# Kernel tuning notes

Measured on AMD Instinct MI355X. Metric: run time of the kernel, lower is better.

The kernel has to match this reference:

```python
import jax, jax.numpy as jnp
import numpy as np
from jax import lax

B, S, CIN, COUT, K = 32, 2048, 256, 256, 16


def setup_inputs() -> dict:
    key = jax.random.key(0)
    k1, k2, k3, k4 = jax.random.split(key, 4)
    x = jax.random.normal(k1, (B, S, CIN), dtype=jnp.float32)
    w_real = jax.random.normal(k2, (COUT, CIN, K), dtype=jnp.float32) * 0.1
    w_imag = jax.random.normal(k3, (COUT, CIN, K), dtype=jnp.float32) * 0.1
    phases = jax.random.normal(k4, (K,), dtype=jnp.float32) * 0.1
    return {"x": x, "w_real": w_real, "w_imag": w_imag, "phases": phases}


def reference(x, w_real, w_imag, phases):
    # out[b,t,o] = Re( sum_{k,i} x[b,t+k,i] * exp(1j*phases[k]) * (w_real + 1j*w_imag)[o,i,k] )
    # x is real, so this equals a real valid conv1d with effective kernel:
    #   w_eff[o,i,k] = cos(phases[k]) * w_real[o,i,k] - sin(phases[k]) * w_imag[o,i,k]
    w_eff = jnp.cos(phases)[None, None, :] * w_real - jnp.sin(phases)[None, None, :] * w_imag
    # conv expects NCH / OIH layouts
    y = lax.conv_general_dilated(
        jnp.transpose(x, (0, 2, 1)),  # [B, CIN, S]
        w_eff,                         # [COUT, CIN, K]
        window_strides=(1,),
        padding="VALID",
        dimension_numbers=("NCH", "OIH", "NCH"),
    )
    return jnp.transpose(y, (0, 2, 1))  # [B, S-K+1, COUT]
```

## Files before the change

kernel.cpp:

```cpp
#include <hip/hip_runtime.h>
#include <math.h>

#define B_    32
#define S_    2048
#define CIN_  256
#define COUT_ 256
#define K_    16
#define TOUT_ 2033
#define RTOT_ 4096

typedef __bf16 bf16x4 __attribute__((ext_vector_type(4)));
typedef __bf16 bf16x8 __attribute__((ext_vector_type(8)));
typedef float  f32x4  __attribute__((ext_vector_type(4)));

#define GLOBAL_AS __attribute__((address_space(1)))
#define LDS_AS    __attribute__((address_space(3)))

__device__ __forceinline__ void gload_lds16(const void* g, void* l) {
  __builtin_amdgcn_global_load_lds((const GLOBAL_AS void*)g, (LDS_AS void*)l, 16, 0, 0);
}

__global__ void __launch_bounds__(256) build_wt_kernel(const float* __restrict__ wr,
                                                       const float* __restrict__ wi,
                                                       const float* __restrict__ ph,
                                                       __bf16* __restrict__ wt) {
  int t = blockIdx.x * 256 + threadIdx.x;
  int o = t >> 8, i = t & 255;
  const float4* wr4 = (const float4*)(wr + (size_t)(o * CIN_ + i) * K_);
  const float4* wi4 = (const float4*)(wi + (size_t)(o * CIN_ + i) * K_);
  float re[16], im[16];
  #pragma unroll
  for (int v = 0; v < 4; v++) {
    float4 a = wr4[v];
    re[4*v+0]=a.x; re[4*v+1]=a.y; re[4*v+2]=a.z; re[4*v+3]=a.w;
    float4 b = wi4[v];
    im[4*v+0]=b.x; im[4*v+1]=b.y; im[4*v+2]=b.z; im[4*v+3]=b.w;
  }
  #pragma unroll
  for (int kk = 0; kk < K_; kk++) {
    float p = ph[kk];
    wt[(size_t)o * RTOT_ + kk * CIN_ + i] = (__bf16)(cosf(p)*re[kk] - sinf(p)*im[kk]);
  }
}

__global__ void __launch_bounds__(256) conv_mfma_kernel(const float* __restrict__ xg,
                                                        const __bf16* __restrict__ wt,
                                                        float* __restrict__ out) {
  __shared__ __align__(16) __bf16 As[144 * 32];
  __shared__ __align__(16) __bf16 Bs[128 * 32];

  const int bx = blockIdx.x;
  const int nb = bx & 1;
  const int mb = (bx >> 1) & 15;
  const int b  = bx >> 5;

  const int tid  = threadIdx.x;
  const int w    = tid >> 6;
  const int lane = tid & 63;
  const int wm   = w >> 1, wn = w & 1;
  const int n16  = lane & 15, q = lane >> 4;

  const int t0 = mb * 128;
  const int o0 = nb * 128;

  const float* xbase = xg + (size_t)b * (S_ * CIN_);

  const int sr = tid >> 3;
  const int sc = (tid & 7) * 4;
  const int br = w * 16 + (lane >> 2);
  const int bc = (lane & 3) * 8;

  f32x4 acc[4][4];
  #pragma unroll
  for (int im_ = 0; im_ < 4; im_++)
    #pragma unroll
    for (int in_ = 0; in_ < 4; in_++)
      acc[im_][in_] = {0.f, 0.f, 0.f, 0.f};

  for (int ic = 0; ic < 8; ++ic) {
    const int i0 = ic * 32;

    __syncthreads();

    {
      const float* xcol = xbase + i0 + sc;
      #pragma unroll
      for (int p = 0; p < 4; p++) {
        int r = p * 32 + sr;
        int rg = t0 + r; rg = (rg < S_) ? rg : (S_ - 1);
        float4 v = *(const float4*)(xcol + (size_t)rg * CIN_);
        bf16x4 o4; o4[0]=(__bf16)v.x; o4[1]=(__bf16)v.y; o4[2]=(__bf16)v.z; o4[3]=(__bf16)v.w;
        *(bf16x4*)(As + r * 32 + sc) = o4;
      }
      if (tid < 128) {
        int r = 128 + sr;
        int rg = t0 + r; rg = (rg < S_) ? rg : (S_ - 1);
        float4 v = *(const float4*)(xcol + (size_t)rg * CIN_);
        bf16x4 o4; o4[0]=(__bf16)v.x; o4[1]=(__bf16)v.y; o4[2]=(__bf16)v.z; o4[3]=(__bf16)v.w;
        *(bf16x4*)(As + r * 32 + sc) = o4;
      }
    }

    for (int kk = 0; kk < K_; ++kk) {
      if (kk) __syncthreads();

      const __bf16* wcol = wt + (size_t)kk * CIN_ + i0 + bc;
      #pragma unroll
      for (int p = 0; p < 2; p++) {
        int orow = o0 + p * 64 + br;
        gload_lds16(wcol + (size_t)orow * RTOT_,
                    (void*)(Bs + (p * 64 + w * 16) * 32));
      }

      __syncthreads();

      bf16x8 af[4], bfrag[4];
      #pragma unroll
      for (int jm = 0; jm < 4; jm++) {
        int row = kk + wm * 64 + jm * 16 + n16;
        af[jm] = *(const bf16x8*)(As + row * 32 + q * 8);
      }
      #pragma unroll
      for (int jn = 0; jn < 4; jn++) {
        int row = wn * 64 + jn * 16 + n16;
        bfrag[jn] = *(const bf16x8*)(Bs + row * 32 + q * 8);
      }
      #pragma unroll
      for (int jm = 0; jm < 4; jm++)
        #pragma unroll
        for (int jn = 0; jn < 4; jn++)
          acc[jm][jn] = __builtin_amdgcn_mfma_f32_16x16x32_bf16(af[jm], bfrag[jn], acc[jm][jn], 0, 0, 0);
    }
  }

  float* obase = out + (size_t)b * TOUT_ * COUT_;
  #pragma unroll
  for (int jm = 0; jm < 4; jm++) {
    #pragma unroll
    for (int r = 0; r < 4; r++) {
      int t = t0 + wm * 64 + jm * 16 + q * 4 + r;
      if (t < TOUT_) {
        float* orow = obase + (size_t)t * COUT_ + o0 + wn * 64 + n16;
        #pragma unroll
        for (int jn = 0; jn < 4; jn++)
          orow[jn * 16] = acc[jm][jn][r];
      }
    }
  }
}

extern "C" void kernel_launch(void* const* d_in, const int* in_sizes, int n_in,
                              void* d_out, int out_size, void* d_ws, size_t ws_size,
                              hipStream_t stream) {
  const float* x  = (const float*)d_in[0];
  const float* wr = (const float*)d_in[1];
  const float* wi = (const float*)d_in[2];
  const float* ph = (const float*)d_in[3];
  float* out = (float*)d_out;

  __bf16* wt = (__bf16*)d_ws;

  build_wt_kernel<<<dim3((COUT_ * CIN_) / 256), dim3(256), 0, stream>>>(wr, wi, ph, wt);
  conv_mfma_kernel<<<dim3(B_ * 16 * 2), dim3(256), 0, stream>>>(x, wt, out);
}
```

Baseline: 230.2 us.

## Pipeline weight tiles through a 4-deep LDS ring with async prefetch

Flattens the channel-chunk and tap loops into one 128-step loop. Weight tiles are prefetched two steps ahead into a 4-buffer LDS ring using global_load_lds, and the two barriers per step become a single hand-written s_waitcnt vmcnt + s_barrier. The aim is to hide weight-load latency behind the MFMA work and cut synchronisation. It also raises MFMA wave priority with s_setprio and asks for 3 blocks per CU through launch bounds. The risks are that hand-counted vmcnt values can be upset by compiler-inserted waits around the input-tile loads, and the larger LDS footprint plus the register cap could cause spills or lower occupancy.

```diff
diff --git a/kernel.cpp b/kernel.cpp
--- a/kernel.cpp
+++ b/kernel.cpp
@@ -43,11 +43,11 @@
   }
 }
 
-__global__ void __launch_bounds__(256) conv_mfma_kernel(const float* __restrict__ xg,
-                                                        const __bf16* __restrict__ wt,
-                                                        float* __restrict__ out) {
+__global__ void __launch_bounds__(256, 3) conv_mfma_kernel(const float* __restrict__ xg,
+                                                           const __bf16* __restrict__ wt,
+                                                           float* __restrict__ out) {
   __shared__ __align__(16) __bf16 As[144 * 32];
-  __shared__ __align__(16) __bf16 Bs[128 * 32];
+  __shared__ __align__(16) __bf16 Bs[4][128 * 32];
 
   const int bx = blockIdx.x;
   const int nb = bx & 1;
@@ -77,59 +77,75 @@
     for (int in_ = 0; in_ < 4; in_++)
       acc[im_][in_] = {0.f, 0.f, 0.f, 0.f};
 
-  for (int ic = 0; ic < 8; ++ic) {
-    const int i0 = ic * 32;
+  auto stage_a = [&](int ic) {
+    const float* xcol = xbase + ic * 32 + sc;
+    #pragma unroll
+    for (int p = 0; p < 4; p++) {
+      int r = p * 32 + sr;
+      int rg = t0 + r; rg = (rg < S_) ? rg : (S_ - 1);
+      float4 v = *(const float4*)(xcol + (size_t)rg * CIN_);
+      bf16x4 o4; o4[0]=(__bf16)v.x; o4[1]=(__bf16)v.y; o4[2]=(__bf16)v.z; o4[3]=(__bf16)v.w;
+      *(bf16x4*)(As + r * 32 + sc) = o4;
+    }
+    if (tid < 128) {
+      int r = 128 + sr;
+      int rg = t0 + r; rg = (rg < S_) ? rg : (S_ - 1);
+      float4 v = *(const float4*)(xcol + (size_t)rg * CIN_);
+      bf16x4 o4; o4[0]=(__bf16)v.x; o4[1]=(__bf16)v.y; o4[2]=(__bf16)v.z; o4[3]=(__bf16)v.w;
+      *(bf16x4*)(As + r * 32 + sc) = o4;
+    }
+  };
 
-    __syncthreads();
+  auto stage_b = [&](int j) {
+    const int kk = j & 15;
+    const int i0 = (j >> 4) * 32;
+    const __bf16* wcol = wt + (size_t)kk * CIN_ + i0 + bc;
+    __bf16* dst = &Bs[j & 3][(w * 16) * 32];
+    #pragma unroll
+    for (int p = 0; p < 2; p++) {
+      int orow = o0 + p * 64 + br;
+      gload_lds16(wcol + (size_t)orow * RTOT_, (void*)(dst + p * 64 * 32));
+    }
+  };
 
-    {
-      const float* xcol = xbase + i0 + sc;
-      #pragma unroll
-      for (int p = 0; p < 4; p++) {
-        int r = p * 32 + sr;
-        int rg = t0 + r; rg = (rg < S_) ? rg : (S_ - 1);
-        float4 v = *(const float4*)(xcol + (size_t)rg * CIN_);
-        bf16x4 o4; o4[0]=(__bf16)v.x; o4[1]=(__bf16)v.y; o4[2]=(__bf16)v.z; o4[3]=(__bf16)v.w;
-        *(bf16x4*)(As + r * 32 + sc) = o4;
-      }
-      if (tid < 128) {
-        int r = 128 + sr;
-        int rg = t0 + r; rg = (rg < S_) ? rg : (S_ - 1);
-        float4 v = *(const float4*)(xcol + (size_t)rg * CIN_);
-        bf16x4 o4; o4[0]=(__bf16)v.x; o4[1]=(__bf16)v.y; o4[2]=(__bf16)v.z; o4[3]=(__bf16)v.w;
-        *(bf16x4*)(As + r * 32 + sc) = o4;
-      }
+  stage_a(0);
+  stage_b(0);
+  stage_b(1);
+  asm volatile("s_waitcnt vmcnt(2) lgkmcnt(0)\n\ts_barrier" ::: "memory");
+
+  for (int j = 0; j < 128; ++j) {
+    if (j + 2 < 128) stage_b(j + 2);
+
+    const int kk = j & 15;
+    const __bf16* bsr = Bs[j & 3];
+    bf16x8 af[4], bfrag[4];
+    #pragma unroll
+    for (int jm = 0; jm < 4; jm++) {
+      int row = kk + wm * 64 + jm * 16 + n16;
+      af[jm] = *(const bf16x8*)(As + row * 32 + q * 8);
+    }
+    #pragma unroll
+    for (int jn = 0; jn < 4; jn++) {
+      int row = wn * 64 + jn * 16 + n16;
+      bfrag[jn] = *(const bf16x8*)(bsr + row * 32 + q * 8);
     }
 
-    for (int kk = 0; kk < K_; ++kk) {
-      if (kk) __syncthreads();
+    __builtin_amdgcn_s_setprio(1);
+    #pragma unroll
+    for (int jm = 0; jm < 4; jm++)
+      #pragma unroll
+      for (int jn = 0; jn < 4; jn++)
+        acc[jm][jn] = __builtin_amdgcn_mfma_f32_16x16x32_bf16(af[jm], bfrag[jn], acc[jm][jn], 0, 0, 0);
+    __builtin_amdgcn_s_setprio(0);
 
-      const __bf16* wcol = wt + (size_t)kk * CIN_ + i0 + bc;
-      #pragma unroll
-      for (int p = 0; p < 2; p++) {
-        int orow = o0 + p * 64 + br;
-        gload_lds16(wcol + (size_t)orow * RTOT_,
-                    (void*)(Bs + (p * 64 + w * 16) * 32));
-      }
+    if (j == 127) break;
 
-      __syncthreads();
+    if (j <= 125) asm volatile("s_waitcnt vmcnt(2)\n\ts_barrier" ::: "memory");
+    else          asm volatile("s_waitcnt vmcnt(0)\n\ts_barrier" ::: "memory");
 
-      bf16x8 af[4], bfrag[4];
-      #pragma unroll
-      for (int jm = 0; jm < 4; jm++) {
-        int row = kk + wm * 64 + jm * 16 + n16;
-        af[jm] = *(const bf16x8*)(As + row * 32 + q * 8);
-      }
-      #pragma unroll
-      for (int jn = 0; jn < 4; jn++) {
-        int row = wn * 64 + jn * 16 + n16;
-        bfrag[jn] = *(const bf16x8*)(Bs + row * 32 + q * 8);
-      }
-      #pragma unroll
-      for (int jm = 0; jm < 4; jm++)
-        #pragma unroll
-        for (int jn = 0; jn < 4; jn++)
-          acc[jm][jn] = __builtin_amdgcn_mfma_f32_16x16x32_bf16(af[jm], bfrag[jn], acc[jm][jn], 0, 0, 0);
+    if ((kk == 15)) {
+      stage_a((j + 1) >> 4);
+      asm volatile("s_waitcnt lgkmcnt(0)\n\ts_barrier" ::: "memory");
     }
   }
 
```

After: 270.0 us. 17.3% more time.
